# Kernel tuning notes

Hardware: AMD Instinct MI355X
Metric: run time of the kernel (lower is better)

Reference implementation:

```python
import jax, jax.numpy as jnp
import numpy as np

# dims: B batch, R seq_num (MSA rows), L seq_len (residues), D emb_dim, C n_emb_2D, H heads
B, R, L, D, C, H = 1, 256, 384, 512, 256, 4
HD = D // H
SCALE = np.float32((HD ** -0.5) / np.sqrt(L))  # head-dim scaling * seqlen_scaling (1/sqrt(L))
EPS = 1e-5


def setup_inputs() -> dict:
    key = jax.random.key(0)
    ks = jax.random.split(key, 6)
    s = 0.02
    return {
        "x": jax.random.normal(ks[0], (B, R, L, D), jnp.float32),
        "pair_feat": jax.random.normal(ks[1], (B, L, L, C), jnp.float32),
        "attn_mask": jnp.ones((B, L), jnp.int32),
        "ln_msa_g": jnp.ones((D,), jnp.float32),
        "ln_msa_b": jnp.zeros((D,), jnp.float32),
        "ln_pair_g": jnp.ones((C,), jnp.float32),
        "ln_pair_b": jnp.zeros((C,), jnp.float32),
        "W_pair": jax.random.normal(ks[2], (C, H), jnp.float32) * s,  # stacked per-head [C,1] linears
        "W_v": jax.random.normal(ks[3], (D, D), jnp.float32) * s,     # stacked per-head [D,HD] value proj
        "W_out": jax.random.normal(ks[4], (D, D), jnp.float32) * s,   # to_out (bias=False)
    }


def _ln(x, g, b):
    mu = jnp.mean(x, axis=-1, keepdims=True)
    var = jnp.mean(jnp.square(x - mu), axis=-1, keepdims=True)
    return (x - mu) * jax.lax.rsqrt(var + EPS) * g + b


def reference(x, pair_feat, attn_mask, ln_msa_g, ln_msa_b, ln_pair_g, ln_pair_b, W_pair, W_v, W_out):
    # MHPair_to_MSA.forward (eval mode, dropout=0)
    msa = _ln(x, ln_msa_g, ln_msa_b)                                  # [B,R,L,D]
    pf = (pair_feat + jnp.swapaxes(pair_feat, 1, 2)) * 0.5            # symmetrize
    pf = _ln(pf, ln_pair_g, ln_pair_b)                                # [B,L,L,C]
    # pair-feature-derived attention logits (no QK^T)
    logits = jnp.einsum('bijc,ch->bhij', pf * SCALE, W_pair)          # [B,H,L,L]
    V = jnp.einsum('brld,de->brle', msa, W_v).reshape(B, R, L, H, HD) # [B,R,L,H,HD]
    mask2 = attn_mask[:, :, None] * attn_mask[:, None, :]             # [B,L,L]
    logits = jnp.where(mask2[:, None, :, :] == 0,
                       jnp.finfo(logits.dtype).min, logits)
    attn = jax.nn.softmax(logits, axis=-1)                            # [B,H,L,L]
    out = jnp.einsum('bhij,brjhd->brihd', attn, V).reshape(B, R, L, D)
    out = out @ W_out                                                 # to_out, bias=False
    return x + out                                                    # residual
```

## Files before the change

### kernel.cpp

```cpp
#include <hip/hip_runtime.h>

#define L_   384
#define D_   512
#define C_   256
#define H_   4
#define RR_  256
#define M1_  98304
#define LL2_ 147456
#define NPAIR_BLOCKS 18480

typedef __bf16 bf16x8 __attribute__((ext_vector_type(8)));
typedef float f32x4 __attribute__((ext_vector_type(4)));

__device__ __forceinline__ unsigned short f2bf_bits(float f) {
  union { float f; unsigned u; } v; v.f = f;
  return (unsigned short)((v.u + 0x7fffu + ((v.u >> 16) & 1u)) >> 16);
}
__device__ __forceinline__ __bf16 f2bf(float f) {
  union { unsigned short s; __bf16 b; } o; o.s = f2bf_bits(f);
  return o.b;
}

__device__ __forceinline__ float wave_sum(float v) {
#pragma unroll
  for (int o = 32; o > 0; o >>= 1) v += __shfl_xor(v, o);
  return v;
}
__device__ __forceinline__ float wave_max(float v) {
#pragma unroll
  for (int o = 32; o > 0; o >>= 1) v = fmaxf(v, __shfl_xor(v, o));
  return v;
}

__global__ __launch_bounds__(256) void ln_msa_kernel(
    const float* __restrict__ x, const float* __restrict__ g,
    const float* __restrict__ b, __bf16* __restrict__ msa) {
  int row = blockIdx.x * 4 + (threadIdx.x >> 6);
  int lane = threadIdx.x & 63;
  const float4* xr = (const float4*)(x + (size_t)row * D_ + lane * 8);
  float4 v0 = xr[0], v1 = xr[1];
  float s1 = v0.x + v0.y + v0.z + v0.w + v1.x + v1.y + v1.z + v1.w;
  float s2 = v0.x * v0.x + v0.y * v0.y + v0.z * v0.z + v0.w * v0.w +
             v1.x * v1.x + v1.y * v1.y + v1.z * v1.z + v1.w * v1.w;
#pragma unroll
  for (int o = 32; o > 0; o >>= 1) {
    s1 += __shfl_xor(s1, o);
    s2 += __shfl_xor(s2, o);
  }
  float mu = s1 * (1.0f / D_);
  float var = s2 * (1.0f / D_) - mu * mu;
  float rs = rsqrtf(var + 1e-5f);
  const float4* gp = (const float4*)(g + lane * 8);
  const float4* bp = (const float4*)(b + lane * 8);
  float4 g0 = gp[0], g1 = gp[1], b0 = bp[0], b1 = bp[1];
  float y[8];
  y[0] = (v0.x - mu) * rs * g0.x + b0.x;
  y[1] = (v0.y - mu) * rs * g0.y + b0.y;
  y[2] = (v0.z - mu) * rs * g0.z + b0.z;
  y[3] = (v0.w - mu) * rs * g0.w + b0.w;
  y[4] = (v1.x - mu) * rs * g1.x + b1.x;
  y[5] = (v1.y - mu) * rs * g1.y + b1.y;
  y[6] = (v1.z - mu) * rs * g1.z + b1.z;
  y[7] = (v1.w - mu) * rs * g1.w + b1.w;
  uint4 pk;
  pk.x = ((unsigned)f2bf_bits(y[1]) << 16) | f2bf_bits(y[0]);
  pk.y = ((unsigned)f2bf_bits(y[3]) << 16) | f2bf_bits(y[2]);
  pk.z = ((unsigned)f2bf_bits(y[5]) << 16) | f2bf_bits(y[4]);
  pk.w = ((unsigned)f2bf_bits(y[7]) << 16) | f2bf_bits(y[6]);
  *(uint4*)(msa + (size_t)row * D_ + lane * 8) = pk;
}

__global__ __launch_bounds__(256) void pair_logits_kernel(
    const float* __restrict__ pf, const int* __restrict__ mask,
    const float* __restrict__ g, const float* __restrict__ b,
    const float* __restrict__ Wp, float* __restrict__ logits) {
  unsigned wid = blockIdx.x * 4 + (threadIdx.x >> 6);
  int lane = threadIdx.x & 63;
  unsigned a = wid / 385u;
  unsigned c = wid - a * 385u;
  int i, j;
  if (c < 384u - a) { i = a; j = a + c; }
  else { i = 383 - a; j = i + (c - (384 - a)); }

  int c0 = lane * 4;
  float4 p1 = *(const float4*)(pf + ((size_t)i * L_ + j) * C_ + c0);
  float4 p2 = *(const float4*)(pf + ((size_t)j * L_ + i) * C_ + c0);
  float4 v;
  v.x = 0.5f * (p1.x + p2.x); v.y = 0.5f * (p1.y + p2.y);
  v.z = 0.5f * (p1.z + p2.z); v.w = 0.5f * (p1.w + p2.w);
  float s1 = v.x + v.y + v.z + v.w;
  float s2 = v.x * v.x + v.y * v.y + v.z * v.z + v.w * v.w;
#pragma unroll
  for (int o = 32; o > 0; o >>= 1) {
    s1 += __shfl_xor(s1, o);
    s2 += __shfl_xor(s2, o);
  }
  float mu = s1 * (1.0f / C_);
  float var = s2 * (1.0f / C_) - mu * mu;
  float rs = rsqrtf(var + 1e-5f);
  float4 gv = *(const float4*)(g + c0);
  float4 bv = *(const float4*)(b + c0);
  float y0 = (v.x - mu) * rs * gv.x + bv.x;
  float y1 = (v.y - mu) * rs * gv.y + bv.y;
  float y2 = (v.z - mu) * rs * gv.z + bv.z;
  float y3 = (v.w - mu) * rs * gv.w + bv.w;
  const float4* wp = (const float4*)Wp;
  float4 w0 = wp[c0], w1 = wp[c0 + 1], w2 = wp[c0 + 2], w3 = wp[c0 + 3];
  float4 t;
  t.x = y0 * w0.x + y1 * w1.x + y2 * w2.x + y3 * w3.x;
  t.y = y0 * w0.y + y1 * w1.y + y2 * w2.y + y3 * w3.y;
  t.z = y0 * w0.z + y1 * w1.z + y2 * w2.z + y3 * w3.z;
  t.w = y0 * w0.w + y1 * w1.w + y2 * w2.w + y3 * w3.w;
#pragma unroll
  for (int o = 32; o > 0; o >>= 1) {
    t.x += __shfl_xor(t.x, o);
    t.y += __shfl_xor(t.y, o);
    t.z += __shfl_xor(t.z, o);
    t.w += __shfl_xor(t.w, o);
  }
  if (lane < 8) {
    int h = lane & 3;
    int ii = (lane < 4) ? i : j;
    int jj = (lane < 4) ? j : i;
    bool ok = (mask[i] != 0) && (mask[j] != 0);
    const float NEG = -3.402823466e38f;
    const float SCALE = (float)(0.08838834764831845 / 19.595917942265423);
    float th = (h == 0) ? t.x : (h == 1) ? t.y : (h == 2) ? t.z : t.w;
    logits[(size_t)h * LL2_ + (size_t)ii * L_ + jj] = ok ? SCALE * th : NEG;
  }
}

__global__ __launch_bounds__(256) void softmax_kernel(
    const float* __restrict__ logits, __bf16* __restrict__ attn) {
  int wave = threadIdx.x >> 6, lane = threadIdx.x & 63;
  int row = blockIdx.x * 4 + wave;
  const float* lr = logits + (size_t)row * L_;
  float v[6];
#pragma unroll
  for (int t = 0; t < 6; ++t) v[t] = lr[lane + t * 64];
  float mx = v[0];
#pragma unroll
  for (int t = 1; t < 6; ++t) mx = fmaxf(mx, v[t]);
  mx = wave_max(mx);
  float s = 0.f;
#pragma unroll
  for (int t = 0; t < 6; ++t) { v[t] = __expf(v[t] - mx); s += v[t]; }
  s = wave_sum(s);
  float inv = 1.0f / s;
  __bf16* ar = attn + (size_t)row * L_;
#pragma unroll
  for (int t = 0; t < 6; ++t) ar[lane + t * 64] = f2bf(v[t] * inv);
}

__global__ __launch_bounds__(256) void wtrans_kernel(
    const float* __restrict__ Wv, const float* __restrict__ Wo,
    __bf16* __restrict__ WvT, __bf16* __restrict__ WoT) {
  int id = blockIdx.x * 256 + threadIdx.x;
  int m = id >> 18;
  int e = (id >> 9) & 511, d = id & 511;
  const float* W = m ? Wo : Wv;
  __bf16* T = m ? WoT : WvT;
  T[(size_t)e * 512 + d] = f2bf(W[(size_t)d * 512 + e]);
}

__device__ __forceinline__ void stage_tile(__bf16* s, const __bf16* g, size_t ld) {
  int tid = threadIdx.x;
#pragma unroll
  for (int it = 0; it < 4; ++it) {
    int cid = it * 256 + tid;
    int row = cid >> 3, chk = cid & 7;
    uint4 v = *(const uint4*)(g + (size_t)row * ld + chk * 8);
    int sb = row * 128 + ((chk * 16) ^ ((row & 7) << 4));
    *(uint4*)((char*)s + sb) = v;
  }
}

__device__ __forceinline__ bf16x8 frag_ld(const __bf16* s, int row, int k) {
  int sb = row * 128 + ((k * 2) ^ ((row & 7) << 4));
  return *(const bf16x8*)((const char*)s + sb);
}

__device__ __forceinline__ void gemm_mainloop(
    const __bf16* __restrict__ Arow, size_t ldA,
    const __bf16* __restrict__ Brow, size_t ldB,
    int K, __bf16* As, __bf16* Bs, f32x4 acc[4][4]) {
  int lane = threadIdx.x & 63, wave = threadIdx.x >> 6;
  int wm = (wave >> 1) * 64, wn = (wave & 1) * 64;
  int fr = lane & 15, fk = (lane >> 4) * 8;
  for (int kt = 0; kt < K; kt += 64) {
    __syncthreads();
    stage_tile(As, Arow + kt, ldA);
    stage_tile(Bs, Brow + kt, ldB);
    __syncthreads();
#pragma unroll
    for (int kk = 0; kk < 2; ++kk) {
      bf16x8 af[4], bfv[4];
#pragma unroll
      for (int mi = 0; mi < 4; ++mi) af[mi] = frag_ld(As, wm + mi * 16 + fr, kk * 32 + fk);
#pragma unroll
      for (int ni = 0; ni < 4; ++ni) bfv[ni] = frag_ld(Bs, wn + ni * 16 + fr, kk * 32 + fk);
#pragma unroll
      for (int mi = 0; mi < 4; ++mi)
#pragma unroll
        for (int ni = 0; ni < 4; ++ni)
          acc[mi][ni] = __builtin_amdgcn_mfma_f32_16x16x32_bf16(af[mi], bfv[ni], acc[mi][ni], 0, 0, 0);
    }
  }
}

__global__ __launch_bounds__(256) void gemm_vt_kernel(
    const __bf16* __restrict__ WvT, const __bf16* __restrict__ msa,
    __bf16* __restrict__ VT) {
  __shared__ __bf16 As[128 * 64], Bs[128 * 64];
  int n0 = blockIdx.x * 128, m0 = blockIdx.y * 128;
  f32x4 acc[4][4] = {};
  gemm_mainloop(WvT + (size_t)m0 * D_, D_, msa + (size_t)n0 * D_, D_, D_, As, Bs, acc);
  int lane = threadIdx.x & 63, wave = threadIdx.x >> 6;
  int wm = (wave >> 1) * 64, wn = (wave & 1) * 64;
  int cr = (lane >> 4) * 4, cc = lane & 15;
#pragma unroll
  for (int mi = 0; mi < 4; ++mi)
#pragma unroll
    for (int ni = 0; ni < 4; ++ni)
#pragma unroll
      for (int rr = 0; rr < 4; ++rr) {
        int row = m0 + wm + mi * 16 + cr + rr;
        int col = n0 + wn + ni * 16 + cc;
        VT[(size_t)row * M1_ + col] = f2bf(acc[mi][ni][rr]);
      }
}

__global__ __launch_bounds__(256) void attnv_kernel(
    const __bf16* __restrict__ attn, const __bf16* __restrict__ VT,
    __bf16* __restrict__ out2) {
  __shared__ __bf16 As[128 * 64], Bs[128 * 64];
  int it = blockIdx.x;
  int rh = blockIdx.y;
  int h = rh & 3, r = rh >> 2;
  const __bf16* A = attn + (size_t)h * LL2_ + (size_t)it * 128 * L_;
  const __bf16* Bt = VT + (size_t)(h * 128) * M1_ + (size_t)r * L_;
  f32x4 acc[4][4] = {};
  gemm_mainloop(A, L_, Bt, M1_, L_, As, Bs, acc);
  int lane = threadIdx.x & 63, wave = threadIdx.x >> 6;
  int wm = (wave >> 1) * 64, wn = (wave & 1) * 64;
  int cr = (lane >> 4) * 4, cc = lane & 15;
#pragma unroll
  for (int mi = 0; mi < 4; ++mi)
#pragma unroll
    for (int ni = 0; ni < 4; ++ni)
#pragma unroll
      for (int rr = 0; rr < 4; ++rr) {
        int row_i = it * 128 + wm + mi * 16 + cr + rr;
        int col = h * 128 + wn + ni * 16 + cc;
        out2[((size_t)r * L_ + row_i) * D_ + col] = f2bf(acc[mi][ni][rr]);
      }
}

__global__ __launch_bounds__(256) void gemm_out_kernel(
    const __bf16* __restrict__ out2, const __bf16* __restrict__ WoT,
    const float* __restrict__ x, float* __restrict__ out) {
  __shared__ __bf16 As[128 * 64], Bs[128 * 64];
  int n0 = blockIdx.x * 128, m0 = blockIdx.y * 128;
  f32x4 acc[4][4] = {};
  gemm_mainloop(out2 + (size_t)m0 * D_, D_, WoT + (size_t)n0 * D_, D_, D_, As, Bs, acc);
  int lane = threadIdx.x & 63, wave = threadIdx.x >> 6;
  int wm = (wave >> 1) * 64, wn = (wave & 1) * 64;
  int cr = (lane >> 4) * 4, cc = lane & 15;
#pragma unroll
  for (int mi = 0; mi < 4; ++mi)
#pragma unroll
    for (int ni = 0; ni < 4; ++ni)
#pragma unroll
      for (int rr = 0; rr < 4; ++rr) {
        int row = m0 + wm + mi * 16 + cr + rr;
        int col = n0 + wn + ni * 16 + cc;
        size_t idx = (size_t)row * D_ + col;
        out[idx] = x[idx] + acc[mi][ni][rr];
      }
}

extern "C" void kernel_launch(void* const* d_in, const int* in_sizes, int n_in,
                              void* d_out, int out_size, void* d_ws, size_t ws_size,
                              hipStream_t stream) {
  const float* x      = (const float*)d_in[0];
  const float* pair   = (const float*)d_in[1];
  const int*   mask   = (const int*)d_in[2];
  const float* g_msa  = (const float*)d_in[3];
  const float* b_msa  = (const float*)d_in[4];
  const float* g_pair = (const float*)d_in[5];
  const float* b_pair = (const float*)d_in[6];
  const float* Wp     = (const float*)d_in[7];
  const float* Wv     = (const float*)d_in[8];
  const float* Wo     = (const float*)d_in[9];
  float* out = (float*)d_out;

  char* p = (char*)d_ws;
  auto alloc = [&](size_t bytes) {
    char* r = p;
    p += (bytes + 255) & ~(size_t)255;
    return r;
  };
  __bf16* msa    = (__bf16*)alloc((size_t)M1_ * D_ * 2);
  __bf16* VT     = (__bf16*)alloc((size_t)D_ * M1_ * 2);
  float*  logits = (float*)alloc((size_t)H_ * LL2_ * 4);
  __bf16* attn   = (__bf16*)alloc((size_t)H_ * LL2_ * 2);
  __bf16* WvT    = (__bf16*)alloc((size_t)512 * 512 * 2);
  __bf16* WoT    = (__bf16*)alloc((size_t)512 * 512 * 2);
  __bf16* out2   = msa;

  wtrans_kernel<<<2048, 256, 0, stream>>>(Wv, Wo, WvT, WoT);
  ln_msa_kernel<<<M1_ / 4, 256, 0, stream>>>(x, g_msa, b_msa, msa);
  gemm_vt_kernel<<<dim3(M1_ / 128, D_ / 128), 256, 0, stream>>>(WvT, msa, VT);
  pair_logits_kernel<<<NPAIR_BLOCKS, 256, 0, stream>>>(pair, mask, g_pair, b_pair, Wp, logits);
  softmax_kernel<<<(H_ * L_) / 4, 256, 0, stream>>>(logits, attn);
  attnv_kernel<<<dim3(3, RR_ * H_), 256, 0, stream>>>(attn, VT, out2);
  gemm_out_kernel<<<dim3(D_ / 128, M1_ / 128), 256, 0, stream>>>(out2, WoT, x, out);
}
```

Baseline: 392.9 us.

## Stage GEMM tiles with direct global-to-LDS loads and XCD-aware block swizzle

Replaces the register round-trip tile staging in the shared GEMM mainloop with global_load_lds direct-to-LDS 16-byte loads. The XOR swizzle moves from the LDS destination to the global source address, so the LDS layout stays the same. All three GEMM kernels also remap block IDs so that consecutive blocks on the same XCD share operand tiles, which should improve L2 reuse. The aim is to cut VGPR traffic and staging instructions and to reduce cross-XCD cache misses. The risk is that the loads still sit behind a plain __syncthreads without explicit vmcnt waits, which may not guarantee the async LDS writes have completed.

```diff
diff --git a/kernel.cpp b/kernel.cpp
--- a/kernel.cpp
+++ b/kernel.cpp
@@ -163,15 +163,20 @@
   T[(size_t)e * 512 + d] = f2bf(W[(size_t)d * 512 + e]);
 }
 
-__device__ __forceinline__ void stage_tile(__bf16* s, const __bf16* g, size_t ld) {
+__device__ __forceinline__ void gload16(const void* g, void* l) {
+  __builtin_amdgcn_global_load_lds(
+      (const __attribute__((address_space(1))) void*)g,
+      (__attribute__((address_space(3))) void*)l, 16, 0, 0);
+}
+
+__device__ __forceinline__ void stage_tile_async(__bf16* s, const __bf16* g, size_t ld) {
   int tid = threadIdx.x;
 #pragma unroll
   for (int it = 0; it < 4; ++it) {
     int cid = it * 256 + tid;
     int row = cid >> 3, chk = cid & 7;
-    uint4 v = *(const uint4*)(g + (size_t)row * ld + chk * 8);
-    int sb = row * 128 + ((chk * 16) ^ ((row & 7) << 4));
-    *(uint4*)((char*)s + sb) = v;
+    int src_off = (chk * 16) ^ ((row & 7) << 4);
+    gload16(g + (size_t)row * ld + (src_off >> 1), (char*)s + cid * 16);
   }
 }
 
@@ -189,8 +194,8 @@
   int fr = lane & 15, fk = (lane >> 4) * 8;
   for (int kt = 0; kt < K; kt += 64) {
     __syncthreads();
-    stage_tile(As, Arow + kt, ldA);
-    stage_tile(Bs, Brow + kt, ldB);
+    stage_tile_async(As, Arow + kt, ldA);
+    stage_tile_async(Bs, Brow + kt, ldB);
     __syncthreads();
 #pragma unroll
     for (int kk = 0; kk < 2; ++kk) {
@@ -206,13 +211,19 @@
           acc[mi][ni] = __builtin_amdgcn_mfma_f32_16x16x32_bf16(af[mi], bfv[ni], acc[mi][ni], 0, 0, 0);
     }
   }
+}
+
+__device__ __forceinline__ unsigned xcd_swz_3072(unsigned bid) {
+  return (bid & 7u) * 384u + (bid >> 3);
 }
 
 __global__ __launch_bounds__(256) void gemm_vt_kernel(
     const __bf16* __restrict__ WvT, const __bf16* __restrict__ msa,
     __bf16* __restrict__ VT) {
   __shared__ __bf16 As[128 * 64], Bs[128 * 64];
-  int n0 = blockIdx.x * 128, m0 = blockIdx.y * 128;
+  unsigned swz = xcd_swz_3072(blockIdx.x + 4 * blockIdx.y);
+  int m0 = (swz & 3) * 128;
+  int n0 = (swz >> 2) * 128;
   f32x4 acc[4][4] = {};
   gemm_mainloop(WvT + (size_t)m0 * D_, D_, msa + (size_t)n0 * D_, D_, D_, As, Bs, acc);
   int lane = threadIdx.x & 63, wave = threadIdx.x >> 6;
@@ -234,8 +245,9 @@
     const __bf16* __restrict__ attn, const __bf16* __restrict__ VT,
     __bf16* __restrict__ out2) {
   __shared__ __bf16 As[128 * 64], Bs[128 * 64];
-  int it = blockIdx.x;
-  int rh = blockIdx.y;
+  unsigned swz = xcd_swz_3072(blockIdx.x + 3 * blockIdx.y);
+  int it = swz % 3u;
+  int rh = swz / 3u;
   int h = rh & 3, r = rh >> 2;
   const __bf16* A = attn + (size_t)h * LL2_ + (size_t)it * 128 * L_;
   const __bf16* Bt = VT + (size_t)(h * 128) * M1_ + (size_t)r * L_;
@@ -260,7 +272,9 @@
     const __bf16* __restrict__ out2, const __bf16* __restrict__ WoT,
     const float* __restrict__ x, float* __restrict__ out) {
   __shared__ __bf16 As[128 * 64], Bs[128 * 64];
-  int n0 = blockIdx.x * 128, m0 = blockIdx.y * 128;
+  unsigned swz = xcd_swz_3072(blockIdx.x + 4 * blockIdx.y);
+  int n0 = (swz & 3) * 128;
+  int m0 = (swz >> 2) * 128;
   f32x4 acc[4][4] = {};
   gemm_mainloop(out2 + (size_t)m0 * D_, D_, WoT + (size_t)n0 * D_, D_, D_, As, Bs, acc);
   int lane = threadIdx.x & 63, wave = threadIdx.x >> 6;
@@ -310,9 +324,9 @@
 
   wtrans_kernel<<<2048, 256, 0, stream>>>(Wv, Wo, WvT, WoT);
   ln_msa_kernel<<<M1_ / 4, 256, 0, stream>>>(x, g_msa, b_msa, msa);
-  gemm_vt_kernel<<<dim3(M1_ / 128, D_ / 128), 256, 0, stream>>>(WvT, msa, VT);
+  gemm_vt_kernel<<<dim3(4, M1_ / 128), 256, 0, stream>>>(WvT, msa, VT);
   pair_logits_kernel<<<NPAIR_BLOCKS, 256, 0, stream>>>(pair, mask, g_pair, b_pair, Wp, logits);
   softmax_kernel<<<(H_ * L_) / 4, 256, 0, stream>>>(logits, attn);
   attnv_kernel<<<dim3(3, RR_ * H_), 256, 0, stream>>>(attn, VT, out2);
-  gemm_out_kernel<<<dim3(D_ / 128, M1_ / 128), 256, 0, stream>>>(out2, WoT, x, out);
-}
+  gemm_out_kernel<<<dim3(4, M1_ / 128), 256, 0, stream>>>(out2, WoT, x, out);
+}
```

Result: faster. 384.5 us (-2.1%).
